# Kernel tuning notes

Measured on AMD Instinct MI355X. Metric: run time of the kernel, lower is better.

The kernel has to match this reference:

```python
import jax, jax.numpy as jnp
import numpy as np

DIM = 768
HEADS = 12
HIDDEN = 4 * DIM
EPS = 1e-5


def _layer_norm(x, g, b):
    mu = jnp.mean(x, axis=-1, keepdims=True)
    var = jnp.mean(jnp.square(x - mu), axis=-1, keepdims=True)
    return (x - mu) * jax.lax.rsqrt(var + EPS) * g + b


def setup_inputs() -> dict:
    key = jax.random.key(0)
    ks = jax.random.split(key, 10)
    B, N, C = 16, 1024, DIM
    s = lambda fan: 1.0 / np.sqrt(fan)
    return {
        "x": jax.random.normal(ks[0], (B, N, C), dtype=jnp.float32),
        "ln1_g": jnp.ones((C,), jnp.float32),
        "ln1_b": jnp.zeros((C,), jnp.float32),
        "qkv_w": jax.random.normal(ks[1], (C, 3 * C), jnp.float32) * s(C),
        "qkv_b": jnp.zeros((3 * C,), jnp.float32),
        "proj_w": jax.random.normal(ks[2], (C, C), jnp.float32) * s(C),
        "proj_b": jnp.zeros((C,), jnp.float32),
        "ln2_g": jnp.ones((C,), jnp.float32),
        "ln2_b": jnp.zeros((C,), jnp.float32),
        "fc1_w": jax.random.normal(ks[3], (C, HIDDEN), jnp.float32) * s(C),
        "fc1_b": jnp.zeros((HIDDEN,), jnp.float32),
        "fc2_w": jax.random.normal(ks[4], (HIDDEN, C), jnp.float32) * s(HIDDEN),
        "fc2_b": jnp.zeros((C,), jnp.float32),
    }


def reference(x, ln1_g, ln1_b, qkv_w, qkv_b, proj_w, proj_b,
              ln2_g, ln2_b, fc1_w, fc1_b, fc2_w, fc2_b):
    B, N, C = x.shape
    Hd = C // HEADS
    scale = Hd ** -0.5

    # --- attention branch (pre-norm) ---
    h = _layer_norm(x, ln1_g, ln1_b)
    qkv = h @ qkv_w + qkv_b                       # [B,N,3C]
    qkv = qkv.reshape(B, N, 3, HEADS, Hd).transpose(2, 0, 3, 1, 4)
    q, k, v = qkv[0], qkv[1], qkv[2]              # [B,H,N,Hd]
    attn = jnp.einsum("bhqd,bhkd->bhqk", q, k) * scale
    attn = jax.nn.softmax(attn, axis=-1)
    o = jnp.einsum("bhqk,bhkd->bhqd", attn, v)    # [B,H,N,Hd]
    o = o.transpose(0, 2, 1, 3).reshape(B, N, C)
    x = x + (o @ proj_w + proj_b)

    # --- MLP branch (pre-norm) ---
    h = _layer_norm(x, ln2_g, ln2_b)
    h = jax.nn.gelu(h @ fc1_w + fc1_b, approximate=False)
    x = x + (h @ fc2_w + fc2_b)
    return x
```

## Files before the change

### kernel.cpp

```cpp
#include <hip/hip_runtime.h>

typedef __bf16 bf16x8 __attribute__((ext_vector_type(8)));
typedef __bf16 bf16x4 __attribute__((ext_vector_type(4)));
typedef float f32x4 __attribute__((ext_vector_type(4)));
typedef float f32x16 __attribute__((ext_vector_type(16)));

#define MFMA16(a,b,c) __builtin_amdgcn_mfma_f32_16x16x32_bf16((a),(b),(c),0,0,0)
#define MFMA32(a,b,c) __builtin_amdgcn_mfma_f32_32x32x16_bf16((a),(b),(c),0,0,0)
#define EXP2R(x) __builtin_amdgcn_exp2f(x)

#define BB   16
#define SEQ  1024
#define CD   768
#define NHD  12
#define HDD  64
#define HID  3072
#define MT   (BB*SEQ)

__device__ __forceinline__ void gload16(const void* g, void* l) {
    __builtin_amdgcn_global_load_lds(
        (const __attribute__((address_space(1))) void*)g,
        (__attribute__((address_space(3))) void*)l, 16, 0, 0);
}

__device__ __forceinline__ unsigned pk2(float lo, float hi) {
    unsigned short a = __builtin_bit_cast(unsigned short, (__bf16)lo);
    unsigned short b = __builtin_bit_cast(unsigned short, (__bf16)hi);
    return (unsigned)a | ((unsigned)b << 16);
}

__device__ __forceinline__ float fast_gelu(float x) {
    float u = x * x * x;
    float y = fmaf(0.044715f, u, x);
    float e = EXP2R(-2.3022083f * y);
    return x * __builtin_amdgcn_rcpf(1.0f + e);
}

__global__ __launch_bounds__(256)
void transpose_w(const float* __restrict__ W, __bf16* __restrict__ WT, int R, int C)
{
    __shared__ float t[32][33];
    int tc = C >> 5;
    int bid = blockIdx.x;
    int br = bid / tc, bc = bid % tc;
    int x = threadIdx.x & 31, y = threadIdx.x >> 5;
#pragma unroll
    for (int i = 0; i < 4; ++i)
        t[y + 8*i][x] = W[(size_t)(br*32 + y + 8*i)*C + bc*32 + x];
    __syncthreads();
#pragma unroll
    for (int i = 0; i < 4; ++i)
        WT[(size_t)(bc*32 + y + 8*i)*R + br*32 + x] = (__bf16)t[x][y + 8*i];
}

__global__ __launch_bounds__(256)
void ln_kernel(const float* __restrict__ xin, const float* __restrict__ g,
               const float* __restrict__ bb, __bf16* out)
{
    int row = blockIdx.x * 4 + (threadIdx.x >> 6);
    int lane = threadIdx.x & 63;
    const float* xr = xin + (size_t)row * CD + lane * 4;
    float4 v0 = *(const float4*)(xr);
    float4 v1 = *(const float4*)(xr + 256);
    float4 v2 = *(const float4*)(xr + 512);
    float s = v0.x+v0.y+v0.z+v0.w + v1.x+v1.y+v1.z+v1.w + v2.x+v2.y+v2.z+v2.w;
#pragma unroll
    for (int off = 1; off < 64; off <<= 1) s += __shfl_xor(s, off);
    float mu = s * (1.0f/768.0f);
    float q =
        (v0.x-mu)*(v0.x-mu)+(v0.y-mu)*(v0.y-mu)+(v0.z-mu)*(v0.z-mu)+(v0.w-mu)*(v0.w-mu)+
        (v1.x-mu)*(v1.x-mu)+(v1.y-mu)*(v1.y-mu)+(v1.z-mu)*(v1.z-mu)+(v1.w-mu)*(v1.w-mu)+
        (v2.x-mu)*(v2.x-mu)+(v2.y-mu)*(v2.y-mu)+(v2.z-mu)*(v2.z-mu)+(v2.w-mu)*(v2.w-mu);
#pragma unroll
    for (int off = 1; off < 64; off <<= 1) q += __shfl_xor(q, off);
    float rstd = rsqrtf(q * (1.0f/768.0f) + 1e-5f);

    __bf16* orow = out + (size_t)row * CD + lane * 4;
#pragma unroll
    for (int p = 0; p < 3; ++p) {
        float4 xv = (p == 0) ? v0 : (p == 1) ? v1 : v2;
        float4 gv = *(const float4*)(g  + p*256 + lane*4);
        float4 bv = *(const float4*)(bb + p*256 + lane*4);
        bf16x4 ov;
        ov[0] = (__bf16)((xv.x-mu)*rstd*gv.x + bv.x);
        ov[1] = (__bf16)((xv.y-mu)*rstd*gv.y + bv.y);
        ov[2] = (__bf16)((xv.z-mu)*rstd*gv.z + bv.z);
        ov[3] = (__bf16)((xv.w-mu)*rstd*gv.w + bv.w);
        *(bf16x4*)(orow + p*256) = ov;
    }
}

template<int EPI>
__global__ __launch_bounds__(256)
void gemm_bt(const __bf16* __restrict__ A, const __bf16* __restrict__ BT,
             const float* __restrict__ bias,
             const float* res, float* outf,
             __bf16* __restrict__ outb,
             __bf16* __restrict__ qb, __bf16* __restrict__ kb, __bf16* __restrict__ vb,
             int M, int N, int K)
{
    __shared__ alignas(16) __bf16 lsA[2][128*64];
    __shared__ alignas(16) __bf16 lsB[2][128*64];

    int nbn = N >> 7;
    int nwg = (M >> 7) * nbn;
    int bid = (int)blockIdx.x;
    int cpx = nwg >> 3;
    int sw = (bid & 7) * cpx + (bid >> 3);
    int bm = sw / nbn, bn = sw % nbn;
    int row0 = bm << 7, col0 = bn << 7;

    int tid = threadIdx.x;
    int lane = tid & 63, w = tid >> 6;
    int wr = w >> 1, wc = w & 1;
    int lr = lane & 15, lg = lane >> 4;

    f32x4 acc[4][4] = {};
    int sbase = w * 4096 + lane * 16;
    int swz = (lr & 7) << 4;

    auto stage = [&](int buf, int ktE) {
#pragma unroll
        for (int i = 0; i < 4; ++i) {
            int s = sbase + (i << 10);
            int r = s >> 7;
            int ch = ((s >> 4) & 7) ^ (r & 7);
            gload16(A  + (size_t)(row0 + r)*K + (ktE + ch*8),
                    (char*)lsA + buf*16384 + (w*4 + i)*1024);
            gload16(BT + (size_t)(col0 + r)*K + (ktE + ch*8),
                    (char*)lsB + buf*16384 + (w*4 + i)*1024);
        }
    };

    int nkt = K >> 6;
    stage(0, 0);

    for (int kt = 0; kt < nkt; ++kt) {
        int cur = kt & 1;
        if (kt + 1 < nkt) {
            stage(cur ^ 1, (kt + 1) << 6);
            asm volatile("s_waitcnt vmcnt(8)" ::: "memory");
        } else {
            asm volatile("s_waitcnt vmcnt(0)" ::: "memory");
        }
        __builtin_amdgcn_s_barrier();

        const char* lA = (const char*)lsA + cur*16384;
        const char* lB = (const char*)lsB + cur*16384;
#pragma unroll
        for (int ks = 0; ks < 2; ++ks) {
            int cb = (ks*64 + lg*16) ^ swz;
            bf16x8 af[4], bfv[4];
#pragma unroll
            for (int m = 0; m < 4; ++m) {
                af[m]  = *(const bf16x8*)(lA + (wr*64 + m*16 + lr)*128 + cb);
                bfv[m] = *(const bf16x8*)(lB + (wc*64 + m*16 + lr)*128 + cb);
            }
#pragma unroll
            for (int m = 0; m < 4; ++m)
#pragma unroll
                for (int n = 0; n < 4; ++n)
                    acc[m][n] = MFMA16(af[m], bfv[n], acc[m][n]);
        }
        asm volatile("s_waitcnt lgkmcnt(0)" ::: "memory");
        __builtin_amdgcn_sched_barrier(0);
        __builtin_amdgcn_s_barrier();
    }

    int rbase = row0 + wr*64 + lg*4;
    int cbase = col0 + wc*64 + lr;
#pragma unroll
    for (int n = 0; n < 4; ++n) {
        int col = cbase + n*16;
        float bv = bias[col];
        if constexpr (EPI == 0) {
            int which = col / CD;
            int c2 = col - which * CD;
            int head = c2 >> 6, d = c2 & 63;
#pragma unroll
            for (int m = 0; m < 4; ++m) {
                int r0 = rbase + m*16;
                int b = r0 >> 10, nn = r0 & 1023;
                if (which == 2) {
                    bf16x4 pv;
#pragma unroll
                    for (int j = 0; j < 4; ++j) pv[j] = (__bf16)(acc[m][n][j] + bv);
                    *(bf16x4*)&vb[(((size_t)b*NHD + head)*HDD + d)*SEQ + nn] = pv;
                } else {
                    __bf16* dst = (which == 0) ? qb : kb;
#pragma unroll
                    for (int j = 0; j < 4; ++j)
                        dst[(((size_t)b*NHD + head)*SEQ + nn + j)*HDD + d] =
                            (__bf16)(acc[m][n][j] + bv);
                }
            }
        } else {
#pragma unroll
            for (int m = 0; m < 4; ++m) {
                int rr = rbase + m*16;
#pragma unroll
                for (int j = 0; j < 4; ++j) {
                    float val = acc[m][n][j] + bv;
                    int r = rr + j;
                    if constexpr (EPI == 1) {
                        outf[(size_t)r*N + col] = res[(size_t)r*N + col] + val;
                    } else {
                        outb[(size_t)r*N + col] = (__bf16)fast_gelu(val);
                    }
                }
            }
        }
    }
}

__global__ __launch_bounds__(256)
void attn_kernel(const __bf16* __restrict__ q, const __bf16* __restrict__ k,
                 const __bf16* __restrict__ vT, __bf16* __restrict__ o)
{
    __shared__ alignas(16) __bf16 kls[2][64*64];
    __shared__ alignas(16) __bf16 vls[2][64*64];

    int bid = blockIdx.x;
    int bh = bid % (BB*NHD);
    int qt = bid / (BB*NHD);
    int b = bh / NHD, hh = bh % NHD;
    int tid = threadIdx.x, lane = tid & 63, w = tid >> 6;
    int lq = lane & 31, h = lane >> 5;

    int qg = qt*128 + w*32 + lq;
    const __bf16* qp = q + ((size_t)bh*SEQ + qg)*HDD + h*8;
    bf16x8 qf[4];
#pragma unroll
    for (int s = 0; s < 4; ++s) qf[s] = *(const bf16x8*)(qp + s*16);

    const __bf16* kbase = k  + (size_t)bh*SEQ*HDD;
    const __bf16* vbase = vT + (size_t)bh*HDD*SEQ;

    int srow0 = tid >> 3;
    int scol0 = ((tid & 7) ^ (srow0 & 7)) * 8;
    int srow1 = srow0 + 32;

    auto stage = [&](int buf, int kv) {
        char* kl = (char*)kls + buf*8192 + w*1024;
        char* vl = (char*)vls + buf*8192 + w*1024;
        gload16(kbase + (size_t)(kv + srow0)*HDD + scol0, kl);
        gload16(kbase + (size_t)(kv + srow1)*HDD + scol0, kl + 4096);
        gload16(vbase + (size_t)srow0*SEQ + kv + scol0, vl);
        gload16(vbase + (size_t)srow1*SEQ + kv + scol0, vl + 4096);
    };

    const float SCL2 = 0.125f * 1.44269504f;
    float mrun = -1e30f, lrun = 0.f;
    f32x16 oa0 = {}, oa1 = {};

    stage(0, 0);
    int rswz = (lq & 7) << 4;

    for (int kt = 0; kt < SEQ/64; ++kt) {
        int cur = kt & 1;
        if (kt + 1 < SEQ/64) {
            stage(cur ^ 1, (kt + 1)*64);
            asm volatile("s_waitcnt vmcnt(4)" ::: "memory");
        } else {
            asm volatile("s_waitcnt vmcnt(0)" ::: "memory");
        }
        __builtin_amdgcn_s_barrier();

        const char* kc = (const char*)kls + cur*8192;
        const char* vc = (const char*)vls + cur*8192;

        bf16x8 ka0[4], ka1[4];
#pragma unroll
        for (int s = 0; s < 4; ++s) {
            int bc = (h*16 + s*32) ^ rswz;
            ka0[s] = *(const bf16x8*)(kc + lq*128 + bc);
            ka1[s] = *(const bf16x8*)(kc + (lq + 32)*128 + bc);
        }
        bf16x8 vf0[4], vf1[4];
#pragma unroll
        for (int g = 0; g < 4; ++g) {
            int bc = (h*16 + g*32) ^ rswz;
            vf0[g] = *(const bf16x8*)(vc + lq*128 + bc);
            vf1[g] = *(const bf16x8*)(vc + (lq + 32)*128 + bc);
        }

        f32x16 s0 = {}, s1 = {};
        __builtin_amdgcn_s_setprio(1);
#pragma unroll
        for (int s = 0; s < 4; ++s) {
            s0 = MFMA32(ka0[s], qf[s], s0);
            s1 = MFMA32(ka1[s], qf[s], s1);
        }
        __builtin_amdgcn_s_setprio(0);

        float t8[8];
#pragma unroll
        for (int i = 0; i < 8; ++i)
            t8[i] = fmaxf(fmaxf(s0[i], s0[i + 8]), fmaxf(s1[i], s1[i + 8]));
        float t4a = fmaxf(fmaxf(t8[0], t8[1]), fmaxf(t8[2], t8[3]));
        float t4b = fmaxf(fmaxf(t8[4], t8[5]), fmaxf(t8[6], t8[7]));
        float tm = fmaxf(t4a, t4b);
        tm = fmaxf(tm, __shfl_xor(tm, 32));
        if (!__all(tm <= mrun)) {
            float mnew = fmaxf(mrun, tm);
            float alpha = EXP2R((mrun - mnew) * SCL2);
            mrun = mnew;
            lrun *= alpha;
            oa0 = oa0 * alpha;
            oa1 = oa1 * alpha;
        }
        float nb = -mrun * SCL2;
#pragma unroll
        for (int i = 0; i < 16; ++i) s0[i] = EXP2R(fmaf(s0[i], SCL2, nb));
#pragma unroll
        for (int i = 0; i < 16; ++i) s1[i] = EXP2R(fmaf(s1[i], SCL2, nb));
        float a8[8];
#pragma unroll
        for (int i = 0; i < 8; ++i)
            a8[i] = (s0[i] + s0[i + 8]) + (s1[i] + s1[i + 8]);
        float s4a = (a8[0] + a8[1]) + (a8[2] + a8[3]);
        float s4b = (a8[4] + a8[5]) + (a8[6] + a8[7]);
        float ts = s4a + s4b;
        ts += __shfl_xor(ts, 32);
        lrun += ts;

#pragma unroll
        for (int t = 0; t < 2; ++t) {
            const f32x16& sp = t ? s1 : s0;
            unsigned d0 = pk2(sp[ 0], sp[ 1]);
            unsigned d1 = pk2(sp[ 2], sp[ 3]);
            unsigned d2 = pk2(sp[ 4], sp[ 5]);
            unsigned d3 = pk2(sp[ 6], sp[ 7]);
            unsigned d4 = pk2(sp[ 8], sp[ 9]);
            unsigned d5 = pk2(sp[10], sp[11]);
            unsigned d6 = pk2(sp[12], sp[13]);
            unsigned d7 = pk2(sp[14], sp[15]);
            unsigned pd0 = __shfl_xor(d0, 32), pd1 = __shfl_xor(d1, 32);
            unsigned pd2 = __shfl_xor(d2, 32), pd3 = __shfl_xor(d3, 32);
            unsigned pd4 = __shfl_xor(d4, 32), pd5 = __shfl_xor(d5, 32);
            unsigned pd6 = __shfl_xor(d6, 32), pd7 = __shfl_xor(d7, 32);
            union { unsigned u[4]; bf16x8 v; } f0, f1;
            f0.u[0] = h ? pd2 : d0;
            f0.u[1] = h ? pd3 : d1;
            f0.u[2] = h ? d2 : pd0;
            f0.u[3] = h ? d3 : pd1;
            f1.u[0] = h ? pd6 : d4;
            f1.u[1] = h ? pd7 : d5;
            f1.u[2] = h ? d6 : pd4;
            f1.u[3] = h ? d7 : pd5;
            __builtin_amdgcn_s_setprio(1);
            oa0 = MFMA32(vf0[t*2 + 0], f0.v, oa0);
            oa1 = MFMA32(vf1[t*2 + 0], f0.v, oa1);
            oa0 = MFMA32(vf0[t*2 + 1], f1.v, oa0);
            oa1 = MFMA32(vf1[t*2 + 1], f1.v, oa1);
            __builtin_amdgcn_s_setprio(0);
        }

        asm volatile("s_waitcnt lgkmcnt(0)" ::: "memory");
        __builtin_amdgcn_sched_barrier(0);
        __builtin_amdgcn_s_barrier();
    }

    float inv = __builtin_amdgcn_rcpf(lrun);
    oa0 = oa0 * inv;
    oa1 = oa1 * inv;
    __bf16* orow = o + ((size_t)b*SEQ + qg)*CD + hh*HDD;
#pragma unroll
    for (int dt = 0; dt < 2; ++dt) {
        f32x16 oa = dt ? oa1 : oa0;
        unsigned d0 = pk2(oa[ 0], oa[ 1]);
        unsigned d1 = pk2(oa[ 2], oa[ 3]);
        unsigned d2 = pk2(oa[ 4], oa[ 5]);
        unsigned d3 = pk2(oa[ 6], oa[ 7]);
        unsigned d4 = pk2(oa[ 8], oa[ 9]);
        unsigned d5 = pk2(oa[10], oa[11]);
        unsigned d6 = pk2(oa[12], oa[13]);
        unsigned d7 = pk2(oa[14], oa[15]);
        unsigned pd0 = __shfl_xor(d0, 32), pd1 = __shfl_xor(d1, 32);
        unsigned pd2 = __shfl_xor(d2, 32), pd3 = __shfl_xor(d3, 32);
        unsigned pd4 = __shfl_xor(d4, 32), pd5 = __shfl_xor(d5, 32);
        unsigned pd6 = __shfl_xor(d6, 32), pd7 = __shfl_xor(d7, 32);
        union { unsigned u[4]; bf16x8 v; } g0, g1;
        g0.u[0] = h ? pd2 : d0;
        g0.u[1] = h ? pd3 : d1;
        g0.u[2] = h ? d2 : pd0;
        g0.u[3] = h ? d3 : pd1;
        g1.u[0] = h ? pd6 : d4;
        g1.u[1] = h ? pd7 : d5;
        g1.u[2] = h ? d6 : pd4;
        g1.u[3] = h ? d7 : pd5;
        *(bf16x8*)(orow + dt*32 +  0 + h*8) = g0.v;
        *(bf16x8*)(orow + dt*32 + 16 + h*8) = g1.v;
    }
}

extern "C" void kernel_launch(void* const* d_in, const int* in_sizes, int n_in,
                              void* d_out, int out_size, void* d_ws, size_t ws_size,
                              hipStream_t stream)
{
    const float* x     = (const float*)d_in[0];
    const float* ln1g  = (const float*)d_in[1];
    const float* ln1b  = (const float*)d_in[2];
    const float* qkvw  = (const float*)d_in[3];
    const float* qkvb  = (const float*)d_in[4];
    const float* projw = (const float*)d_in[5];
    const float* projb = (const float*)d_in[6];
    const float* ln2g  = (const float*)d_in[7];
    const float* ln2b  = (const float*)d_in[8];
    const float* fc1w  = (const float*)d_in[9];
    const float* fc1b  = (const float*)d_in[10];
    const float* fc2w  = (const float*)d_in[11];
    const float* fc2b  = (const float*)d_in[12];
    float* out = (float*)d_out;

    char* p = (char*)d_ws;
    auto alloc = [&](size_t bytes) { char* r = p; p += (bytes + 255) & ~(size_t)255; return r; };
    __bf16* wqkvT  = (__bf16*)alloc((size_t)3*CD*CD*2);
    __bf16* wprojT = (__bf16*)alloc((size_t)CD*CD*2);
    __bf16* wfc1T  = (__bf16*)alloc((size_t)HID*CD*2);
    __bf16* wfc2T  = (__bf16*)alloc((size_t)CD*HID*2);
    __bf16* hbuf   = (__bf16*)alloc((size_t)MT*CD*2);
    __bf16* qbuf   = (__bf16*)alloc((size_t)BB*NHD*SEQ*HDD*2);
    __bf16* kbuf   = (__bf16*)alloc((size_t)BB*NHD*SEQ*HDD*2);
    __bf16* vtbuf  = (__bf16*)alloc((size_t)BB*NHD*SEQ*HDD*2);
    (void)alloc((size_t)BB*NHD*SEQ*HDD*2);
    __bf16* hhbuf  = qbuf;

    transpose_w<<<(CD/32)*(3*CD/32), 256, 0, stream>>>(qkvw,  wqkvT, CD, 3*CD);
    transpose_w<<<(CD/32)*(CD/32),   256, 0, stream>>>(projw, wprojT, CD, CD);
    transpose_w<<<(CD/32)*(HID/32),  256, 0, stream>>>(fc1w,  wfc1T, CD, HID);
    transpose_w<<<(HID/32)*(CD/32),  256, 0, stream>>>(fc2w,  wfc2T, HID, CD);

    ln_kernel<<<MT/4, 256, 0, stream>>>(x, ln1g, ln1b, hbuf);

    gemm_bt<0><<<(MT/128)*(3*CD/128), 256, 0, stream>>>(
        hbuf, wqkvT, qkvb, nullptr, nullptr, nullptr, qbuf, kbuf, vtbuf, MT, 3*CD, CD);

    attn_kernel<<<BB*NHD*8, 256, 0, stream>>>(qbuf, kbuf, vtbuf, hbuf);

    gemm_bt<1><<<(MT/128)*(CD/128), 256, 0, stream>>>(
        hbuf, wprojT, projb, x, out, nullptr, nullptr, nullptr, nullptr, MT, CD, CD);

    ln_kernel<<<MT/4, 256, 0, stream>>>(out, ln2g, ln2b, hbuf);

    gemm_bt<2><<<(MT/128)*(HID/128), 256, 0, stream>>>(
        hbuf, wfc1T, fc1b, nullptr, nullptr, hhbuf, nullptr, nullptr, nullptr, MT, HID, CD);

    gemm_bt<1><<<(MT/128)*(CD/128), 256, 0, stream>>>(
        hhbuf, wfc2T, fc2b, out, out, nullptr, nullptr, nullptr, nullptr, MT, CD, HID);
}
```

Measured before the change: 519.6 us.

## Load GEMM B operand directly from global and simplify pipeline synchronization

The GEMM kernel no longer stages the B (weight) tile through LDS. Each wave reads its B fragments straight from global memory into registers, which halves LDS usage and drops the B LDS reads. The hand-tuned vmcnt waits and barriers are replaced with __syncthreads in both the GEMM and attention loops. The direct loads are strided per row and are issued without overlap ahead of the MFMAs, so they add global-memory latency and lose coalescing. The simpler barriers may also serialize the prefetch against compute.

```diff
diff --git a/kernel.cpp b/kernel.cpp
--- a/kernel.cpp
+++ b/kernel.cpp
@@ -100,7 +100,6 @@
              int M, int N, int K)
 {
     __shared__ alignas(16) __bf16 lsA[2][128*64];
-    __shared__ alignas(16) __bf16 lsB[2][128*64];
 
     int nbn = N >> 7;
     int nwg = (M >> 7) * nbn;
@@ -119,52 +118,49 @@
     int sbase = w * 4096 + lane * 16;
     int swz = (lr & 7) << 4;
 
-    auto stage = [&](int buf, int ktE) {
+    auto stageA = [&](int buf, int ktE) {
 #pragma unroll
         for (int i = 0; i < 4; ++i) {
             int s = sbase + (i << 10);
             int r = s >> 7;
             int ch = ((s >> 4) & 7) ^ (r & 7);
-            gload16(A  + (size_t)(row0 + r)*K + (ktE + ch*8),
+            gload16(A + (size_t)(row0 + r)*K + (ktE + ch*8),
                     (char*)lsA + buf*16384 + (w*4 + i)*1024);
-            gload16(BT + (size_t)(col0 + r)*K + (ktE + ch*8),
-                    (char*)lsB + buf*16384 + (w*4 + i)*1024);
         }
     };
 
+    const __bf16* bp = BT + (size_t)(col0 + wc*64 + lr)*K + lg*8;
+
     int nkt = K >> 6;
-    stage(0, 0);
+    stageA(0, 0);
+    __syncthreads();
 
     for (int kt = 0; kt < nkt; ++kt) {
         int cur = kt & 1;
-        if (kt + 1 < nkt) {
-            stage(cur ^ 1, (kt + 1) << 6);
-            asm volatile("s_waitcnt vmcnt(8)" ::: "memory");
-        } else {
-            asm volatile("s_waitcnt vmcnt(0)" ::: "memory");
-        }
-        __builtin_amdgcn_s_barrier();
+        if (kt + 1 < nkt) stageA(cur ^ 1, (kt + 1) << 6);
 
         const char* lA = (const char*)lsA + cur*16384;
-        const char* lB = (const char*)lsB + cur*16384;
+        int ke = kt << 6;
+        bf16x8 bf0[4], bf1[4];
+#pragma unroll
+        for (int m = 0; m < 4; ++m) {
+            bf0[m] = *(const bf16x8*)(bp + (size_t)m*16*K + ke);
+            bf1[m] = *(const bf16x8*)(bp + (size_t)m*16*K + ke + 32);
+        }
 #pragma unroll
         for (int ks = 0; ks < 2; ++ks) {
             int cb = (ks*64 + lg*16) ^ swz;
-            bf16x8 af[4], bfv[4];
-#pragma unroll
-            for (int m = 0; m < 4; ++m) {
-                af[m]  = *(const bf16x8*)(lA + (wr*64 + m*16 + lr)*128 + cb);
-                bfv[m] = *(const bf16x8*)(lB + (wc*64 + m*16 + lr)*128 + cb);
-            }
+            bf16x8 af[4];
 #pragma unroll
             for (int m = 0; m < 4; ++m)
+                af[m] = *(const bf16x8*)(lA + (wr*64 + m*16 + lr)*128 + cb);
+#pragma unroll
+            for (int m = 0; m < 4; ++m)
 #pragma unroll
                 for (int n = 0; n < 4; ++n)
-                    acc[m][n] = MFMA16(af[m], bfv[n], acc[m][n]);
-        }
-        asm volatile("s_waitcnt lgkmcnt(0)" ::: "memory");
-        __builtin_amdgcn_sched_barrier(0);
-        __builtin_amdgcn_s_barrier();
+                    acc[m][n] = MFMA16(af[m], ks ? bf1[n] : bf0[n], acc[m][n]);
+        }
+        __syncthreads();
     }
 
     int rbase = row0 + wr*64 + lg*4;
@@ -254,17 +250,12 @@
     f32x16 oa0 = {}, oa1 = {};
 
     stage(0, 0);
+    __syncthreads();
+    int cur = 0;
     int rswz = (lq & 7) << 4;
 
     for (int kt = 0; kt < SEQ/64; ++kt) {
-        int cur = kt & 1;
-        if (kt + 1 < SEQ/64) {
-            stage(cur ^ 1, (kt + 1)*64);
-            asm volatile("s_waitcnt vmcnt(4)" ::: "memory");
-        } else {
-            asm volatile("s_waitcnt vmcnt(0)" ::: "memory");
-        }
-        __builtin_amdgcn_s_barrier();
+        if (kt + 1 < SEQ/64) stage(cur ^ 1, (kt + 1)*64);
 
         const char* kc = (const char*)kls + cur*8192;
         const char* vc = (const char*)vls + cur*8192;
@@ -356,9 +347,8 @@
             __builtin_amdgcn_s_setprio(0);
         }
 
-        asm volatile("s_waitcnt lgkmcnt(0)" ::: "memory");
-        __builtin_amdgcn_sched_barrier(0);
-        __builtin_amdgcn_s_barrier();
+        __syncthreads();
+        cur ^= 1;
     }
 
     float inv = __builtin_amdgcn_rcpf(lrun);
```

Result: slower. 790.2 us (+52.1%).
